# Optimization experiments

Measured on AMD Instinct MI355X. Metric: run time of the kernel, lower is better.

The kernel has to match this reference:

```python
import jax, jax.numpy as jnp
import numpy as np

B, T, RNN_DIM, EMB_DIM, ATT_DIM = 64, 2048, 1024, 512, 128
N_FILT, KSIZE = 32, 31
PAD = (KSIZE - 1) // 2


def setup_inputs() -> dict:
    key = jax.random.key(0)
    ks = jax.random.split(key, 9)
    return {
        "attention_hidden_state": jax.random.normal(ks[0], (B, RNN_DIM), jnp.float32),
        "memory": jax.random.normal(ks[1], (B, T, EMB_DIM), jnp.float32),
        "processed_memory": jax.random.normal(ks[2], (B, T, ATT_DIM), jnp.float32),
        "attention_weights_cat": jax.random.uniform(ks[3], (B, 2, T), jnp.float32),
        "mask": jnp.zeros((B, T), dtype=bool),
        # learned params (torch Linear stores weight as (out, in))
        "Wq": jax.random.normal(ks[4], (ATT_DIM, RNN_DIM), jnp.float32) * 0.02,
        "conv_w": jax.random.normal(ks[5], (N_FILT, 2, KSIZE), jnp.float32) * 0.1,
        "Wd": jax.random.normal(ks[6], (ATT_DIM, N_FILT), jnp.float32) * 0.1,
        "v": jax.random.normal(ks[7], (1, ATT_DIM), jnp.float32) * 0.1,
    }


def reference(attention_hidden_state, memory, processed_memory,
              attention_weights_cat, mask, Wq, conv_w, Wd, v):
    # processed_query: (B, 1, ATT_DIM)
    pq = jnp.einsum('br,ar->ba', attention_hidden_state, Wq)[:, None, :]
    # location conv: (B, 2, T) -> (B, N_FILT, T), padding keeps length
    loc = jax.lax.conv_general_dilated(
        attention_weights_cat, conv_w,
        window_strides=(1,), padding=[(PAD, PAD)],
        dimension_numbers=('NCH', 'OIH', 'NCH'))
    # transpose to (B, T, N_FILT), dense to (B, T, ATT_DIM)
    loc = jnp.einsum('bft,af->bta', loc, Wd)
    # energies: tanh(pq + loc + pm) @ v^T -> (B, T)
    energies = jnp.einsum('bta,a->bt', jnp.tanh(pq + loc + processed_memory), v[0])
    energies = jnp.where(mask, -jnp.inf, energies)
    attention_weights = jax.nn.softmax(energies, axis=1)
    # context: (B, 1, T) x (B, T, EMB) -> (B, EMB)
    attention_context = jnp.einsum('bt,bte->be', attention_weights, memory)
    return attention_context, attention_weights
```

## Files before the change

### kernel.cpp

```cpp
#include <hip/hip_runtime.h>
#include <hip/hip_bf16.h>
#include <cstdint>

#define BB 64
#define TN 2048
#define RNN 1024
#define EMB 512
#define ATT 128
#define NF 32
#define KS 31
#define PADK 15
#define CKN 62
#define ETT 256
#define NCHUNK 16
#define CHT 128

__device__ __forceinline__ float fast_rcp(float x) {
#if __has_builtin(__builtin_amdgcn_rcpf)
    return __builtin_amdgcn_rcpf(x);
#else
    return 1.0f / x;
#endif
}

__device__ __forceinline__ float fast_tanh(float x) {
    float s = __expf(2.0f * x);
    return 1.0f - 2.0f * fast_rcp(s + 1.0f);
}

__global__ __launch_bounds__(256) void prep_kernel(
    const float* __restrict__ ahs, const float* __restrict__ Wq,
    const float* __restrict__ conv_w, const float* __restrict__ Wd,
    float* __restrict__ ws_pq, float* __restrict__ ws_UT)
{
    int tid = threadIdx.x;
    if (blockIdx.x < BB) {
        int b = blockIdx.x;
        __shared__ float sh[RNN];
        for (int i = tid; i < RNN; i += 256) sh[i] = ahs[b * RNN + i];
        __syncthreads();
        int a = tid & 127, half = tid >> 7;
        const float4* wq4 = (const float4*)(Wq + a * RNN + half * (RNN / 2));
        const float4* sh4 = (const float4*)(sh + half * (RNN / 2));
        float acc = 0.0f;
#pragma unroll 8
        for (int i = 0; i < RNN / 8; ++i) {
            float4 w4 = wq4[i]; float4 h4 = sh4[i];
            acc = fmaf(w4.x, h4.x, acc);
            acc = fmaf(w4.y, h4.y, acc);
            acc = fmaf(w4.z, h4.z, acc);
            acc = fmaf(w4.w, h4.w, acc);
        }
        __shared__ float part[256];
        part[tid] = acc;
        __syncthreads();
        if (half == 0) ws_pq[b * ATT + a] = part[a] + part[a + 128];
    } else {
        __shared__ float sWd[ATT * NF];
        __shared__ float sCw[NF * CKN];
        for (int i = tid; i < ATT * NF; i += 256) sWd[i] = Wd[i];
        for (int i = tid; i < NF * CKN; i += 256) sCw[i] = conv_w[i];
        __syncthreads();
        for (int idx = tid; idx < ATT * CKN; idx += 256) {
            int a = idx & 127, ck = idx >> 7;
            float acc = 0.0f;
#pragma unroll
            for (int f = 0; f < NF; ++f) acc = fmaf(sWd[a * NF + f], sCw[f * CKN + ck], acc);
            ws_UT[idx] = acc;
        }
    }
}

__global__ __launch_bounds__(256) void energies_kernel(
    const float* __restrict__ awc, const float* __restrict__ pm,
    const float* __restrict__ vvec,
    const float* __restrict__ ws_pq, const float* __restrict__ ws_UT,
    float* __restrict__ ws_e)
{
    __shared__ float sA[2][ETT + 32];
    __shared__ float sE[2][ETT];
    int tid = threadIdx.x;
    int b = blockIdx.x, t0 = blockIdx.y * ETT;

    for (int idx = tid; idx < 2 * (ETT + 30); idx += 256) {
        int c = idx / (ETT + 30), tt = idx % (ETT + 30);
        int t = t0 + tt - PADK;
        sA[c][tt] = (t >= 0 && t < TN) ? awc[(b * 2 + c) * TN + t] : 0.0f;
    }

    int lane = tid & 63, w = tid >> 6;
    int h = w & 1, seg = w >> 1;
    int a = h * 64 + lane;

    float U[CKN];
#pragma unroll
    for (int k = 0; k < CKN; ++k) U[k] = ws_UT[k * ATT + a];
    float q = ws_pq[b * ATT + a];
    float vv = vvec[a];
    const float* pmb = pm + (size_t)b * TN * ATT + a;
    __syncthreads();

    int tbeg = seg * (ETT / 2);
    for (int tl = tbeg; tl < tbeg + ETT / 2; tl += 4) {
        float xw0[34], xw1[34];
#pragma unroll
        for (int j = 0; j < 34; ++j) {
            xw0[j] = sA[0][tl + j];
            xw1[j] = sA[1][tl + j];
        }
        float p[4];
#pragma unroll
        for (int u = 0; u < 4; ++u)
            p[u] = pmb[(size_t)(t0 + tl + u) * ATT];
#pragma unroll
        for (int u = 0; u < 4; ++u) {
            float lo = 0.0f;
#pragma unroll
            for (int k = 0; k < KS; ++k) {
                lo = fmaf(U[k],      xw0[u + k], lo);
                lo = fmaf(U[KS + k], xw1[u + k], lo);
            }
            float e = vv * fast_tanh(q + lo + p[u]);
#pragma unroll
            for (int off = 32; off >= 1; off >>= 1) e += __shfl_xor(e, off, 64);
            if (lane == 0) sE[h][tl + u] = e;
        }
    }
    __syncthreads();
    ws_e[b * TN + t0 + tid] = sE[0][tid] + sE[1][tid];
}

__global__ __launch_bounds__(256) void context_fused_kernel(
    const float* __restrict__ ws_e, const uint8_t* __restrict__ mask,
    const float* __restrict__ mem,
    float* __restrict__ out_w, float* __restrict__ partial)
{
    int b = blockIdx.x, ch = blockIdx.y, tid = threadIdx.x;

    float vals[TN / 256];
    float m = -INFINITY;
#pragma unroll
    for (int i = 0; i < TN / 256; ++i) {
        int t = tid + i * 256;
        float e = ws_e[b * TN + t];
        if (mask[b * TN + t]) e = -INFINITY;
        vals[i] = e;
        m = fmaxf(m, e);
    }
    __shared__ float redm[4];
#pragma unroll
    for (int off = 32; off >= 1; off >>= 1) m = fmaxf(m, __shfl_xor(m, off, 64));
    if ((tid & 63) == 0) redm[tid >> 6] = m;
    __syncthreads();
    m = fmaxf(fmaxf(redm[0], redm[1]), fmaxf(redm[2], redm[3]));

    float s = 0.0f;
#pragma unroll
    for (int i = 0; i < TN / 256; ++i) s += __expf(vals[i] - m);
    __shared__ float reds[4];
#pragma unroll
    for (int off = 32; off >= 1; off >>= 1) s += __shfl_xor(s, off, 64);
    if ((tid & 63) == 0) reds[tid >> 6] = s;
    __syncthreads();
    s = reds[0] + reds[1] + reds[2] + reds[3];
    float inv = 1.0f / s;

    __shared__ float sw[CHT];
    int tc0 = ch * CHT;
    if (tid < CHT) {
        int t = tc0 + tid;
        float e = ws_e[b * TN + t];
        if (mask[b * TN + t]) e = -INFINITY;
        float wgt = __expf(e - m) * inv;
        out_w[b * TN + t] = wgt;
        sw[tid] = wgt;
    }
    __syncthreads();

    int e4 = tid & 127, sub = tid >> 7;
    const float4* m4 = (const float4*)(mem + ((size_t)(b * TN + tc0)) * EMB);
    float4 acc = make_float4(0.f, 0.f, 0.f, 0.f);
    for (int i = sub; i < CHT; i += 2) {
        float wt = sw[i];
        float4 mv = m4[(size_t)i * 128 + e4];
        acc.x = fmaf(wt, mv.x, acc.x);
        acc.y = fmaf(wt, mv.y, acc.y);
        acc.z = fmaf(wt, mv.z, acc.z);
        acc.w = fmaf(wt, mv.w, acc.w);
    }
    __shared__ float4 sacc[128];
    if (sub == 1) sacc[e4] = acc;
    __syncthreads();
    if (sub == 0) {
        float4 o = sacc[e4];
        acc.x += o.x; acc.y += o.y; acc.z += o.z; acc.w += o.w;
        ((float4*)partial)[((size_t)ch * BB + b) * 128 + e4] = acc;
    }
}

__global__ __launch_bounds__(256) void context_reduce_kernel(
    const float* __restrict__ partial, float* __restrict__ out_ctx)
{
    int o = blockIdx.x * 256 + threadIdx.x;
    int b = o >> 9, e = o & 511;
    float acc = 0.0f;
#pragma unroll
    for (int c = 0; c < NCHUNK; ++c)
        acc += partial[((size_t)c * BB + b) * EMB + e];
    out_ctx[o] = acc;
}

extern "C" void kernel_launch(void* const* d_in, const int* in_sizes, int n_in,
                              void* d_out, int out_size, void* d_ws, size_t ws_size,
                              hipStream_t stream) {
    const float*   ahs  = (const float*)d_in[0];
    const float*   mem  = (const float*)d_in[1];
    const float*   pm   = (const float*)d_in[2];
    const float*   awc  = (const float*)d_in[3];
    const uint8_t* mask = (const uint8_t*)d_in[4];
    const float*   Wq   = (const float*)d_in[5];
    const float*   cw   = (const float*)d_in[6];
    const float*   Wd   = (const float*)d_in[7];
    const float*   v    = (const float*)d_in[8];

    float* out_ctx = (float*)d_out;
    float* out_w   = (float*)d_out + BB * EMB;

    float* ws      = (float*)d_ws;
    float* ws_pq   = ws;
    float* ws_UT   = ws + 8192;
    float* ws_e    = ws + 16384;
    float* ws_part = ws + 147456;

    prep_kernel<<<BB + 1, 256, 0, stream>>>(ahs, Wq, cw, Wd, ws_pq, ws_UT);
    energies_kernel<<<dim3(BB, TN / ETT), 256, 0, stream>>>(awc, pm, v, ws_pq, ws_UT, ws_e);
    context_fused_kernel<<<dim3(BB, NCHUNK), 256, 0, stream>>>(ws_e, mask, mem, out_w, ws_part);
    context_reduce_kernel<<<(BB * EMB) / 256, 256, 0, stream>>>(ws_part, out_ctx);
}
```

Measured before the change: 477.0 us.

## Fuse energies, online softmax and context accumulation into one flash-style kernel

Merges energy computation with an online (running max/sum) softmax and the weighted memory accumulation, so each tile block computes energies for 32-step chunks and immediately accumulates context partials, rescaling by a running max. Separate small kernels then combine per-tile max/sum to produce final weights and the normalized context. This removes the standalone context kernel's redundant per-block softmax over all of T and overlaps memory streaming with compute, at the cost of more syncthreads per chunk and serialized exp work per thread. The sA reads are also vectorized to float4.

```diff
diff --git a/kernel.cpp b/kernel.cpp
--- a/kernel.cpp
+++ b/kernel.cpp
@@ -12,8 +12,8 @@
 #define PADK 15
 #define CKN 62
 #define ETT 256
-#define NCHUNK 16
-#define CHT 128
+#define CHK 32
+#define NTILE (TN / ETT)
 
 __device__ __forceinline__ float fast_rcp(float x) {
 #if __has_builtin(__builtin_amdgcn_rcpf)
@@ -71,16 +71,21 @@
     }
 }
 
-__global__ __launch_bounds__(256) void energies_kernel(
+__global__ __launch_bounds__(256) void fused_kernel(
     const float* __restrict__ awc, const float* __restrict__ pm,
-    const float* __restrict__ vvec,
+    const float* __restrict__ vvec, const uint8_t* __restrict__ mask,
+    const float* __restrict__ mem,
     const float* __restrict__ ws_pq, const float* __restrict__ ws_UT,
-    float* __restrict__ ws_e)
-{
-    __shared__ float sA[2][ETT + 32];
-    __shared__ float sE[2][ETT];
+    float* __restrict__ ws_e, float* __restrict__ ws_mt,
+    float* __restrict__ ws_st, float* __restrict__ ws_cpart)
+{
+    __shared__ __align__(16) float sA[2][ETT + 32];
+    __shared__ float sEc[2][CHK];
+    __shared__ float sEsum[CHK];
+    __shared__ float4 sacc[128];
+
     int tid = threadIdx.x;
-    int b = blockIdx.x, t0 = blockIdx.y * ETT;
+    int b = blockIdx.x, tile = blockIdx.y, t0 = tile * ETT;
 
     for (int idx = tid; idx < 2 * (ETT + 30); idx += 256) {
         int c = idx / (ETT + 30), tt = idx % (ETT + 30);
@@ -98,116 +103,122 @@
     float q = ws_pq[b * ATT + a];
     float vv = vvec[a];
     const float* pmb = pm + (size_t)b * TN * ATT + a;
+    const float4* m4 = (const float4*)(mem + (size_t)(b * TN + t0) * EMB);
+    int e4 = tid & 127, sub = tid >> 7;
+
+    float m_run = -1e30f, s_run = 0.0f;
+    float4 acc = make_float4(0.f, 0.f, 0.f, 0.f);
     __syncthreads();
 
-    int tbeg = seg * (ETT / 2);
-    for (int tl = tbeg; tl < tbeg + ETT / 2; tl += 4) {
-        float xw0[34], xw1[34];
-#pragma unroll
-        for (int j = 0; j < 34; ++j) {
-            xw0[j] = sA[0][tl + j];
-            xw1[j] = sA[1][tl + j];
-        }
-        float p[4];
-#pragma unroll
-        for (int u = 0; u < 4; ++u)
-            p[u] = pmb[(size_t)(t0 + tl + u) * ATT];
-#pragma unroll
-        for (int u = 0; u < 4; ++u) {
-            float lo = 0.0f;
-#pragma unroll
-            for (int k = 0; k < KS; ++k) {
-                lo = fmaf(U[k],      xw0[u + k], lo);
-                lo = fmaf(U[KS + k], xw1[u + k], lo);
+    for (int c = 0; c < ETT / CHK; ++c) {
+        int cb = c * CHK;
+#pragma unroll
+        for (int g = 0; g < 4; ++g) {
+            int tl = cb + seg * 16 + g * 4;
+            const float4* a0 = (const float4*)(&sA[0][tl]);
+            const float4* a1 = (const float4*)(&sA[1][tl]);
+            float x0[36], x1[36];
+#pragma unroll
+            for (int j = 0; j < 9; ++j) {
+                float4 r0 = a0[j], r1 = a1[j];
+                x0[4 * j] = r0.x; x0[4 * j + 1] = r0.y; x0[4 * j + 2] = r0.z; x0[4 * j + 3] = r0.w;
+                x1[4 * j] = r1.x; x1[4 * j + 1] = r1.y; x1[4 * j + 2] = r1.z; x1[4 * j + 3] = r1.w;
             }
-            float e = vv * fast_tanh(q + lo + p[u]);
-#pragma unroll
-            for (int off = 32; off >= 1; off >>= 1) e += __shfl_xor(e, off, 64);
-            if (lane == 0) sE[h][tl + u] = e;
-        }
-    }
-    __syncthreads();
-    ws_e[b * TN + t0 + tid] = sE[0][tid] + sE[1][tid];
-}
-
-__global__ __launch_bounds__(256) void context_fused_kernel(
-    const float* __restrict__ ws_e, const uint8_t* __restrict__ mask,
-    const float* __restrict__ mem,
-    float* __restrict__ out_w, float* __restrict__ partial)
-{
-    int b = blockIdx.x, ch = blockIdx.y, tid = threadIdx.x;
-
-    float vals[TN / 256];
-    float m = -INFINITY;
-#pragma unroll
-    for (int i = 0; i < TN / 256; ++i) {
-        int t = tid + i * 256;
-        float e = ws_e[b * TN + t];
-        if (mask[b * TN + t]) e = -INFINITY;
-        vals[i] = e;
-        m = fmaxf(m, e);
-    }
-    __shared__ float redm[4];
-#pragma unroll
-    for (int off = 32; off >= 1; off >>= 1) m = fmaxf(m, __shfl_xor(m, off, 64));
-    if ((tid & 63) == 0) redm[tid >> 6] = m;
-    __syncthreads();
-    m = fmaxf(fmaxf(redm[0], redm[1]), fmaxf(redm[2], redm[3]));
-
-    float s = 0.0f;
-#pragma unroll
-    for (int i = 0; i < TN / 256; ++i) s += __expf(vals[i] - m);
-    __shared__ float reds[4];
-#pragma unroll
-    for (int off = 32; off >= 1; off >>= 1) s += __shfl_xor(s, off, 64);
-    if ((tid & 63) == 0) reds[tid >> 6] = s;
-    __syncthreads();
-    s = reds[0] + reds[1] + reds[2] + reds[3];
-    float inv = 1.0f / s;
-
-    __shared__ float sw[CHT];
-    int tc0 = ch * CHT;
-    if (tid < CHT) {
-        int t = tc0 + tid;
-        float e = ws_e[b * TN + t];
-        if (mask[b * TN + t]) e = -INFINITY;
-        float wgt = __expf(e - m) * inv;
-        out_w[b * TN + t] = wgt;
-        sw[tid] = wgt;
-    }
-    __syncthreads();
-
-    int e4 = tid & 127, sub = tid >> 7;
-    const float4* m4 = (const float4*)(mem + ((size_t)(b * TN + tc0)) * EMB);
-    float4 acc = make_float4(0.f, 0.f, 0.f, 0.f);
-    for (int i = sub; i < CHT; i += 2) {
-        float wt = sw[i];
-        float4 mv = m4[(size_t)i * 128 + e4];
-        acc.x = fmaf(wt, mv.x, acc.x);
-        acc.y = fmaf(wt, mv.y, acc.y);
-        acc.z = fmaf(wt, mv.z, acc.z);
-        acc.w = fmaf(wt, mv.w, acc.w);
-    }
-    __shared__ float4 sacc[128];
+            float p[4];
+#pragma unroll
+            for (int u = 0; u < 4; ++u) p[u] = pmb[(size_t)(t0 + tl + u) * ATT];
+#pragma unroll
+            for (int u = 0; u < 4; ++u) {
+                float lo = 0.0f;
+#pragma unroll
+                for (int k = 0; k < KS; ++k) {
+                    lo = fmaf(U[k],      x0[u + k], lo);
+                    lo = fmaf(U[KS + k], x1[u + k], lo);
+                }
+                float e = vv * fast_tanh(q + lo + p[u]);
+#pragma unroll
+                for (int off = 32; off >= 1; off >>= 1) e += __shfl_xor(e, off, 64);
+                if (lane == 0) sEc[h][seg * 16 + g * 4 + u] = e;
+            }
+        }
+        __syncthreads();
+        if (tid < CHK) {
+            float e = sEc[0][tid] + sEc[1][tid];
+            if (mask[(size_t)b * TN + t0 + cb + tid]) e = -1e30f;
+            sEsum[tid] = e;
+            ws_e[(size_t)b * TN + t0 + cb + tid] = e;
+        }
+        __syncthreads();
+        float m_new = m_run;
+#pragma unroll
+        for (int i = 0; i < CHK; ++i) m_new = fmaxf(m_new, sEsum[i]);
+        float scl = __expf(m_run - m_new);
+        float s_add = 0.0f;
+#pragma unroll
+        for (int i = 0; i < CHK; ++i) s_add += __expf(sEsum[i] - m_new);
+        s_run = fmaf(s_run, scl, s_add);
+        acc.x *= scl; acc.y *= scl; acc.z *= scl; acc.w *= scl;
+        m_run = m_new;
+        for (int i = sub; i < CHK; i += 2) {
+            float wt = __expf(sEsum[i] - m_new);
+            float4 mv = m4[(size_t)(cb + i) * 128 + e4];
+            acc.x = fmaf(wt, mv.x, acc.x);
+            acc.y = fmaf(wt, mv.y, acc.y);
+            acc.z = fmaf(wt, mv.z, acc.z);
+            acc.w = fmaf(wt, mv.w, acc.w);
+        }
+        __syncthreads();
+    }
+
     if (sub == 1) sacc[e4] = acc;
     __syncthreads();
     if (sub == 0) {
         float4 o = sacc[e4];
         acc.x += o.x; acc.y += o.y; acc.z += o.z; acc.w += o.w;
-        ((float4*)partial)[((size_t)ch * BB + b) * 128 + e4] = acc;
-    }
-}
-
-__global__ __launch_bounds__(256) void context_reduce_kernel(
-    const float* __restrict__ partial, float* __restrict__ out_ctx)
+        ((float4*)&ws_cpart[((size_t)tile * BB + b) * EMB])[e4] = acc;
+        if (tid == 0) {
+            ws_mt[tile * BB + b] = m_run;
+            ws_st[tile * BB + b] = s_run;
+        }
+    }
+}
+
+__global__ __launch_bounds__(256) void weights_kernel(
+    const float* __restrict__ ws_e, const float* __restrict__ ws_mt,
+    const float* __restrict__ ws_st, float* __restrict__ out_w)
+{
+    int b = blockIdx.x, tid = threadIdx.x;
+    float m = -1e30f;
+#pragma unroll
+    for (int t = 0; t < NTILE; ++t) m = fmaxf(m, ws_mt[t * BB + b]);
+    float S = 0.0f;
+#pragma unroll
+    for (int t = 0; t < NTILE; ++t) S += ws_st[t * BB + b] * __expf(ws_mt[t * BB + b] - m);
+    float inv = 1.0f / S;
+#pragma unroll
+    for (int i = 0; i < TN / 256; ++i) {
+        int t = tid + i * 256;
+        out_w[(size_t)b * TN + t] = __expf(ws_e[(size_t)b * TN + t] - m) * inv;
+    }
+}
+
+__global__ __launch_bounds__(256) void ctx_reduce_kernel(
+    const float* __restrict__ ws_cpart, const float* __restrict__ ws_mt,
+    const float* __restrict__ ws_st, float* __restrict__ out_ctx)
 {
     int o = blockIdx.x * 256 + threadIdx.x;
     int b = o >> 9, e = o & 511;
-    float acc = 0.0f;
-#pragma unroll
-    for (int c = 0; c < NCHUNK; ++c)
-        acc += partial[((size_t)c * BB + b) * EMB + e];
-    out_ctx[o] = acc;
+    float m = -1e30f;
+#pragma unroll
+    for (int t = 0; t < NTILE; ++t) m = fmaxf(m, ws_mt[t * BB + b]);
+    float S = 0.0f, acc = 0.0f;
+#pragma unroll
+    for (int t = 0; t < NTILE; ++t) {
+        float f = __expf(ws_mt[t * BB + b] - m);
+        S += ws_st[t * BB + b] * f;
+        acc += ws_cpart[((size_t)t * BB + b) * EMB + e] * f;
+    }
+    out_ctx[o] = acc / S;
 }
 
 extern "C" void kernel_launch(void* const* d_in, const int* in_sizes, int n_in,
@@ -226,14 +237,17 @@
     float* out_ctx = (float*)d_out;
     float* out_w   = (float*)d_out + BB * EMB;
 
-    float* ws      = (float*)d_ws;
-    float* ws_pq   = ws;
-    float* ws_UT   = ws + 8192;
-    float* ws_e    = ws + 16384;
-    float* ws_part = ws + 147456;
+    float* ws       = (float*)d_ws;
+    float* ws_pq    = ws;
+    float* ws_UT    = ws + 8192;
+    float* ws_e     = ws + 16384;
+    float* ws_mt    = ws + 147456;
+    float* ws_st    = ws + 147968;
+    float* ws_cpart = ws + 148480;
 
     prep_kernel<<<BB + 1, 256, 0, stream>>>(ahs, Wq, cw, Wd, ws_pq, ws_UT);
-    energies_kernel<<<dim3(BB, TN / ETT), 256, 0, stream>>>(awc, pm, v, ws_pq, ws_UT, ws_e);
-    context_fused_kernel<<<dim3(BB, NCHUNK), 256, 0, stream>>>(ws_e, mask, mem, out_w, ws_part);
-    context_reduce_kernel<<<(BB * EMB) / 256, 256, 0, stream>>>(ws_part, out_ctx);
-}
+    fused_kernel<<<dim3(BB, NTILE), 256, 0, stream>>>(
+        awc, pm, v, mask, mem, ws_pq, ws_UT, ws_e, ws_mt, ws_st, ws_cpart);
+    weights_kernel<<<BB, 256, 0, stream>>>(ws_e, ws_mt, ws_st, out_w);
+    ctx_reduce_kernel<<<(BB * EMB) / 256, 256, 0, stream>>>(ws_cpart, ws_mt, ws_st, out_ctx);
+}
```

New measurement: 490.8 us. +2.9%, slower.
